# Optimization experiments

Measured on AMD Instinct MI355X. Metric: run time of the kernel, lower is better.

Reference implementation:

```python
import jax, jax.numpy as jnp
import numpy as np

TEMPERATURE = 0.1
EPS = 1e-08
NEG_INF = -9e15


def setup_inputs() -> dict:
    key = jax.random.key(0)
    k1, k2 = jax.random.split(key)
    B, D = 4096, 256
    z_i = jax.random.normal(k1, (B, D), dtype=jnp.float32)
    z_j = jax.random.normal(k2, (B, D), dtype=jnp.float32)
    mask_positive = jnp.ones((B,), dtype=bool)
    return {"z_i": z_i, "z_j": z_j, "mask_positive": mask_positive}


def reference(z_i, z_j, mask_positive):
    B = z_i.shape[0]
    N = 2 * B
    z = jnp.concatenate([z_i, z_j], axis=0)  # [N, D]
    # cosine similarity: normalize (norms clamped to eps) then GEMM
    norms = jnp.maximum(jnp.linalg.norm(z, axis=1, keepdims=True), EPS)
    zn = z / norms
    sim = jnp.matmul(zn, zn.T) / TEMPERATURE  # [N, N]
    # mask self-similarity on diagonal
    rows = jnp.arange(N)
    sim = sim.at[rows, rows].set(NEG_INF)
    logprob = jax.nn.log_softmax(sim, axis=1)
    # positive of row k is row (k+B) mod N
    positives = jnp.concatenate([jnp.arange(B, N), jnp.arange(0, B)])
    loss_vec = -logprob[rows, positives]  # [N]
    mp = jnp.concatenate([mask_positive, mask_positive])  # [N] bool
    cnt = jnp.sum(mp.astype(jnp.float32))
    total = jnp.sum(jnp.where(mp, loss_vec, 0.0))
    loss = jnp.where(cnt > 0, total / jnp.maximum(cnt, 1.0), 0.0)
    return loss
```

## Files before the change

### kernel.cpp

```cpp
#include <hip/hip_runtime.h>
#include <hip/hip_bf16.h>

#define NTOT   8192
#define BHALF  4096
#define DDIM   256
#define TEMP_INV 10.0f
#define SMOD   16
#define NPART  4

typedef __attribute__((ext_vector_type(8))) short bf16x8_t;
typedef __attribute__((ext_vector_type(4))) float f32x4_t;

__device__ inline unsigned short f2bf(float x) {
    __hip_bfloat16 h = __float2bfloat16(x);
    return __builtin_bit_cast(unsigned short, h);
}

__global__ void norm_pair_kernel(const float* __restrict__ zi,
                                 const float* __restrict__ zj,
                                 unsigned short* __restrict__ zn,
                                 float* __restrict__ posdot,
                                 float* __restrict__ s_part) {
    int gtid = blockIdx.x * 256 + threadIdx.x;
    if (gtid < NTOT * NPART) s_part[gtid] = 0.0f;
    int k    = gtid >> 6;
    int lane = gtid & 63;
    float4 vi = reinterpret_cast<const float4*>(zi + (size_t)k * DDIM)[lane];
    float4 vj = reinterpret_cast<const float4*>(zj + (size_t)k * DDIM)[lane];
    float ssi = vi.x*vi.x + vi.y*vi.y + vi.z*vi.z + vi.w*vi.w;
    float ssj = vj.x*vj.x + vj.y*vj.y + vj.z*vj.z + vj.w*vj.w;
    float dot = vi.x*vj.x + vi.y*vj.y + vi.z*vj.z + vi.w*vj.w;
    #pragma unroll
    for (int off = 32; off >= 1; off >>= 1) {
        ssi += __shfl_xor(ssi, off);
        ssj += __shfl_xor(ssj, off);
        dot += __shfl_xor(dot, off);
    }
    float ri = 1.0f / fmaxf(sqrtf(ssi), 1e-8f);
    float rj = 1.0f / fmaxf(sqrtf(ssj), 1e-8f);
    ushort4 oi, oj;
    oi.x = f2bf(vi.x * ri); oi.y = f2bf(vi.y * ri);
    oi.z = f2bf(vi.z * ri); oi.w = f2bf(vi.w * ri);
    oj.x = f2bf(vj.x * rj); oj.y = f2bf(vj.y * rj);
    oj.z = f2bf(vj.z * rj); oj.w = f2bf(vj.w * rj);
    reinterpret_cast<ushort4*>(zn + (size_t)k * DDIM)[lane] = oi;
    reinterpret_cast<ushort4*>(zn + (size_t)(k + BHALF) * DDIM)[lane] = oj;
    if (lane == 0) posdot[k] = dot * ri * rj * TEMP_INV;
}

__global__ void __launch_bounds__(256)
gemm_sym_kernel(const unsigned short* __restrict__ zn,
                float* __restrict__ s_part) {
    __shared__ unsigned short ldsB[64 * 256];
    __shared__ float colred[4][64];

    const int bi = blockIdx.x;
    const int s  = blockIdx.y;
    const int R0 = bi << 7;

    int cs0 = 2 * bi + ((s - 2 * bi) & (SMOD - 1));
    if (cs0 >= 128) return;

    const int tid  = threadIdx.x;
    const int lane = tid & 63;
    const int wv   = tid >> 6;
    const int m    = lane & 15;
    const int quad = lane >> 4;

    float* rowPart = s_part + (size_t)(s  & (NPART - 1)) * NTOT;
    float* colPart = s_part + (size_t)(bi & (NPART - 1)) * NTOT;

    bf16x8_t afrag[2][8];
    #pragma unroll
    for (int rf = 0; rf < 2; ++rf) {
        const unsigned short* arow = zn + (size_t)(R0 + wv*32 + rf*16 + m) * DDIM;
        #pragma unroll
        for (int kk = 0; kk < 8; ++kk)
            afrag[rf][kk] = *reinterpret_cast<const bf16x8_t*>(arow + kk*32 + quad*8);
    }

    float rowacc[2][4] = {{0.f,0.f,0.f,0.f},{0.f,0.f,0.f,0.f}};

    for (int cs = cs0; cs < 128; cs += SMOD) {
        const int C0 = cs << 6;
        const bool isDiag = ((cs >> 1) == bi);

        #pragma unroll
        for (int t = 0; t < 8; ++t) {
            int ci = t * 256 + tid;
            int r = ci >> 5, c = ci & 31;
            bf16x8_t v = *reinterpret_cast<const bf16x8_t*>(
                             zn + (size_t)(C0 + r) * DDIM + c * 8);
            *reinterpret_cast<bf16x8_t*>(&ldsB[r * 256 + ((c ^ (r & 7)) << 3)]) = v;
        }
        __syncthreads();

        #pragma unroll
        for (int cf = 0; cf < 4; ++cf) {
            f32x4_t cacc0 = (f32x4_t){0.f,0.f,0.f,0.f};
            f32x4_t cacc1 = (f32x4_t){0.f,0.f,0.f,0.f};
            #pragma unroll
            for (int kk = 0; kk < 8; ++kk) {
                bf16x8_t b = *reinterpret_cast<const bf16x8_t*>(
                    &ldsB[(cf*16 + m) * 256 + (((kk*4 + quad) ^ (m & 7)) << 3)]);
                cacc0 = __builtin_amdgcn_mfma_f32_16x16x32_bf16(afrag[0][kk], b, cacc0, 0, 0, 0);
                cacc1 = __builtin_amdgcn_mfma_f32_16x16x32_bf16(afrag[1][kk], b, cacc1, 0, 0, 0);
            }
            const int gc = C0 + cf*16 + m;
            float colsum = 0.f;
            #pragma unroll
            for (int r = 0; r < 4; ++r) {
                int gr0 = R0 + wv*32 + quad*4 + r;
                float e0 = __expf(cacc0[r] * TEMP_INV);
                float e1 = __expf(cacc1[r] * TEMP_INV);
                if (isDiag && gr0 == gc)        e0 = 0.f;
                if (isDiag && (gr0 + 16) == gc) e1 = 0.f;
                rowacc[0][r] += e0;
                rowacc[1][r] += e1;
                colsum += e0 + e1;
            }
            if (!isDiag) {
                colsum += __shfl_xor(colsum, 16);
                colsum += __shfl_xor(colsum, 32);
                if (quad == 0) colred[wv][cf*16 + m] = colsum;
            }
        }
        __syncthreads();

        if (!isDiag && tid < 64)
            atomicAdd(&colPart[C0 + tid],
                      colred[0][tid] + colred[1][tid] + colred[2][tid] + colred[3][tid]);
    }

    #pragma unroll
    for (int rf = 0; rf < 2; ++rf)
        #pragma unroll
        for (int r = 0; r < 4; ++r) {
            float v = rowacc[rf][r];
            v += __shfl_xor(v, 1);
            v += __shfl_xor(v, 2);
            v += __shfl_xor(v, 4);
            v += __shfl_xor(v, 8);
            if (m == 0)
                atomicAdd(&rowPart[R0 + wv*32 + rf*16 + quad*4 + r], v);
        }
}

__global__ void finalize_kernel(const float* __restrict__ s_part,
                                const float* __restrict__ posdot,
                                const unsigned char* __restrict__ mask,
                                float* __restrict__ out) {
    int tid = threadIdx.x, lane = tid & 63, wv = tid >> 6;
    float tot = 0.f, cnt = 0.f;
    #pragma unroll
    for (int si = 0; si < NTOT / 1024; ++si) {
        int k = si * 1024 + tid;
        int kb = k & (BHALF - 1);
        if (mask[kb] != 0) {
            float sk = s_part[k] + s_part[NTOT + k]
                     + s_part[2*NTOT + k] + s_part[3*NTOT + k];
            tot += __logf(sk) - posdot[kb];
            cnt += 1.f;
        }
    }
    #pragma unroll
    for (int off = 32; off >= 1; off >>= 1) {
        tot += __shfl_xor(tot, off);
        cnt += __shfl_xor(cnt, off);
    }
    __shared__ float st[16], sc[16];
    if (lane == 0) { st[wv] = tot; sc[wv] = cnt; }
    __syncthreads();
    if (tid == 0) {
        float T = 0.f, C = 0.f;
        #pragma unroll
        for (int i = 0; i < 16; ++i) { T += st[i]; C += sc[i]; }
        out[0] = (C > 0.f) ? (T / fmaxf(C, 1.f)) : 0.f;
    }
}

extern "C" void kernel_launch(void* const* d_in, const int* in_sizes, int n_in,
                              void* d_out, int out_size, void* d_ws, size_t ws_size,
                              hipStream_t stream) {
    const float* zi = (const float*)d_in[0];
    const float* zj = (const float*)d_in[1];
    const unsigned char* mask = (const unsigned char*)d_in[2];
    float* out = (float*)d_out;

    unsigned short* zn = (unsigned short*)d_ws;
    float* s_part = (float*)((char*)d_ws + (size_t)NTOT * DDIM * 2);
    float* posdot = s_part + NPART * NTOT;

    norm_pair_kernel<<<dim3(1024), dim3(256), 0, stream>>>(zi, zj, zn, posdot, s_part);
    gemm_sym_kernel<<<dim3(64, SMOD), dim3(256), 0, stream>>>(zn, s_part);
    finalize_kernel<<<dim3(1), dim3(1024), 0, stream>>>(s_part, posdot, mask, out);
}
```

Before: 111.1 us.

## Pair complementary row blocks per workgroup and read B fragments directly from global

Each workgroup now handles row block bi and its mirror 63-bi, so the triangular work is spread evenly across half as many workgroups. The LDS staging of the B tile and its per-iteration barriers are removed; B fragments are loaded straight from global memory (through cache) into MFMA operands. Column partial sums are buffered in LDS slots and flushed with atomics after a single barrier at the end. Launch bounds request two workgroups per CU. The cost is redundant global/L2 traffic for B, since each wave now fetches the full B tile itself instead of sharing it through LDS.

```diff
diff --git a/kernel.cpp b/kernel.cpp
--- a/kernel.cpp
+++ b/kernel.cpp
@@ -7,6 +7,7 @@
 #define TEMP_INV 10.0f
 #define SMOD   16
 #define NPART  4
+#define MAXSLOT 9
 
 typedef __attribute__((ext_vector_type(8))) short bf16x8_t;
 typedef __attribute__((ext_vector_type(4))) float f32x4_t;
@@ -48,102 +49,112 @@
     if (lane == 0) posdot[k] = dot * ri * rj * TEMP_INV;
 }
 
-__global__ void __launch_bounds__(256)
+__global__ void __launch_bounds__(256, 2)
 gemm_sym_kernel(const unsigned short* __restrict__ zn,
                 float* __restrict__ s_part) {
-    __shared__ unsigned short ldsB[64 * 256];
-    __shared__ float colred[4][64];
-
-    const int bi = blockIdx.x;
-    const int s  = blockIdx.y;
-    const int R0 = bi << 7;
-
-    int cs0 = 2 * bi + ((s - 2 * bi) & (SMOD - 1));
-    if (cs0 >= 128) return;
+    __shared__ float colLDS[MAXSLOT][4][64];
 
     const int tid  = threadIdx.x;
     const int lane = tid & 63;
     const int wv   = tid >> 6;
     const int m    = lane & 15;
     const int quad = lane >> 4;
-
-    float* rowPart = s_part + (size_t)(s  & (NPART - 1)) * NTOT;
-    float* colPart = s_part + (size_t)(bi & (NPART - 1)) * NTOT;
-
-    bf16x8_t afrag[2][8];
-    #pragma unroll
-    for (int rf = 0; rf < 2; ++rf) {
-        const unsigned short* arow = zn + (size_t)(R0 + wv*32 + rf*16 + m) * DDIM;
-        #pragma unroll
-        for (int kk = 0; kk < 8; ++kk)
-            afrag[rf][kk] = *reinterpret_cast<const bf16x8_t*>(arow + kk*32 + quad*8);
-    }
-
-    float rowacc[2][4] = {{0.f,0.f,0.f,0.f},{0.f,0.f,0.f,0.f}};
-
-    for (int cs = cs0; cs < 128; cs += SMOD) {
-        const int C0 = cs << 6;
-        const bool isDiag = ((cs >> 1) == bi);
-
-        #pragma unroll
-        for (int t = 0; t < 8; ++t) {
-            int ci = t * 256 + tid;
-            int r = ci >> 5, c = ci & 31;
-            bf16x8_t v = *reinterpret_cast<const bf16x8_t*>(
-                             zn + (size_t)(C0 + r) * DDIM + c * 8);
-            *reinterpret_cast<bf16x8_t*>(&ldsB[r * 256 + ((c ^ (r & 7)) << 3)]) = v;
-        }
-        __syncthreads();
-
-        #pragma unroll
-        for (int cf = 0; cf < 4; ++cf) {
-            f32x4_t cacc0 = (f32x4_t){0.f,0.f,0.f,0.f};
-            f32x4_t cacc1 = (f32x4_t){0.f,0.f,0.f,0.f};
+    const int biA  = blockIdx.x;
+    const int s    = blockIdx.y;
+
+    float* rowPart = s_part + (size_t)(s   & (NPART - 1)) * NTOT;
+    float* colPart = s_part + (size_t)(biA & (NPART - 1)) * NTOT;
+
+    int slot = 0;
+    #pragma unroll
+    for (int p = 0; p < 2; ++p) {
+        const int bi = p ? (63 - biA) : biA;
+        const int R0 = bi << 7;
+        const int cs0 = 2 * bi + ((s - 2 * bi) & (SMOD - 1));
+        if (cs0 >= 128) continue;
+
+        bf16x8_t afrag[2][8];
+        #pragma unroll
+        for (int rf = 0; rf < 2; ++rf) {
+            const unsigned short* arow = zn + (size_t)(R0 + wv*32 + rf*16 + m) * DDIM;
             #pragma unroll
-            for (int kk = 0; kk < 8; ++kk) {
-                bf16x8_t b = *reinterpret_cast<const bf16x8_t*>(
-                    &ldsB[(cf*16 + m) * 256 + (((kk*4 + quad) ^ (m & 7)) << 3)]);
-                cacc0 = __builtin_amdgcn_mfma_f32_16x16x32_bf16(afrag[0][kk], b, cacc0, 0, 0, 0);
-                cacc1 = __builtin_amdgcn_mfma_f32_16x16x32_bf16(afrag[1][kk], b, cacc1, 0, 0, 0);
+            for (int kk = 0; kk < 8; ++kk)
+                afrag[rf][kk] = *reinterpret_cast<const bf16x8_t*>(arow + kk*32 + quad*8);
+        }
+
+        float rowacc[2][4] = {{0.f,0.f,0.f,0.f},{0.f,0.f,0.f,0.f}};
+
+        for (int cs = cs0; cs < 128; cs += SMOD) {
+            const int C0 = cs << 6;
+            const bool isDiag = ((cs >> 1) == bi);
+
+            #pragma unroll
+            for (int cf = 0; cf < 4; ++cf) {
+                const unsigned short* bbase =
+                    zn + (size_t)(C0 + cf*16 + m) * DDIM + quad*8;
+                f32x4_t c0 = (f32x4_t){0.f,0.f,0.f,0.f};
+                f32x4_t c1 = (f32x4_t){0.f,0.f,0.f,0.f};
+                #pragma unroll
+                for (int kk = 0; kk < 8; ++kk) {
+                    bf16x8_t b = *reinterpret_cast<const bf16x8_t*>(bbase + kk*32);
+                    c0 = __builtin_amdgcn_mfma_f32_16x16x32_bf16(afrag[0][kk], b, c0, 0, 0, 0);
+                    c1 = __builtin_amdgcn_mfma_f32_16x16x32_bf16(afrag[1][kk], b, c1, 0, 0, 0);
+                }
+                const int gc = C0 + cf*16 + m;
+                float colsum = 0.f;
+                #pragma unroll
+                for (int r = 0; r < 4; ++r) {
+                    int gr0 = R0 + wv*32 + quad*4 + r;
+                    float e0 = __expf(c0[r] * TEMP_INV);
+                    float e1 = __expf(c1[r] * TEMP_INV);
+                    if (isDiag && gr0 == gc)        e0 = 0.f;
+                    if (isDiag && (gr0 + 16) == gc) e1 = 0.f;
+                    rowacc[0][r] += e0;
+                    rowacc[1][r] += e1;
+                    colsum += e0 + e1;
+                }
+                if (!isDiag) {
+                    colsum += __shfl_xor(colsum, 16);
+                    colsum += __shfl_xor(colsum, 32);
+                    if (quad == 0) colLDS[slot][wv][cf*16 + m] = colsum;
+                }
             }
-            const int gc = C0 + cf*16 + m;
-            float colsum = 0.f;
+            ++slot;
+        }
+
+        #pragma unroll
+        for (int rf = 0; rf < 2; ++rf)
             #pragma unroll
             for (int r = 0; r < 4; ++r) {
-                int gr0 = R0 + wv*32 + quad*4 + r;
-                float e0 = __expf(cacc0[r] * TEMP_INV);
-                float e1 = __expf(cacc1[r] * TEMP_INV);
-                if (isDiag && gr0 == gc)        e0 = 0.f;
-                if (isDiag && (gr0 + 16) == gc) e1 = 0.f;
-                rowacc[0][r] += e0;
-                rowacc[1][r] += e1;
-                colsum += e0 + e1;
+                float v = rowacc[rf][r];
+                v += __shfl_xor(v, 1);
+                v += __shfl_xor(v, 2);
+                v += __shfl_xor(v, 4);
+                v += __shfl_xor(v, 8);
+                if (m == 0)
+                    atomicAdd(&rowPart[R0 + wv*32 + rf*16 + quad*4 + r], v);
             }
-            if (!isDiag) {
-                colsum += __shfl_xor(colsum, 16);
-                colsum += __shfl_xor(colsum, 32);
-                if (quad == 0) colred[wv][cf*16 + m] = colsum;
+    }
+
+    __syncthreads();
+
+    if (tid < 64) {
+        int slot2 = 0;
+        #pragma unroll
+        for (int p = 0; p < 2; ++p) {
+            const int bi = p ? (63 - biA) : biA;
+            const int cs0 = 2 * bi + ((s - 2 * bi) & (SMOD - 1));
+            if (cs0 >= 128) continue;
+            for (int cs = cs0; cs < 128; cs += SMOD) {
+                if ((cs >> 1) != bi) {
+                    float v = colLDS[slot2][0][tid] + colLDS[slot2][1][tid]
+                            + colLDS[slot2][2][tid] + colLDS[slot2][3][tid];
+                    atomicAdd(&colPart[(cs << 6) + tid], v);
+                }
+                ++slot2;
             }
         }
-        __syncthreads();
-
-        if (!isDiag && tid < 64)
-            atomicAdd(&colPart[C0 + tid],
-                      colred[0][tid] + colred[1][tid] + colred[2][tid] + colred[3][tid]);
-    }
-
-    #pragma unroll
-    for (int rf = 0; rf < 2; ++rf)
-        #pragma unroll
-        for (int r = 0; r < 4; ++r) {
-            float v = rowacc[rf][r];
-            v += __shfl_xor(v, 1);
-            v += __shfl_xor(v, 2);
-            v += __shfl_xor(v, 4);
-            v += __shfl_xor(v, 8);
-            if (m == 0)
-                atomicAdd(&rowPart[R0 + wv*32 + rf*16 + quad*4 + r], v);
-        }
+    }
 }
 
 __global__ void finalize_kernel(const float* __restrict__ s_part,
@@ -192,6 +203,6 @@
     float* posdot = s_part + NPART * NTOT;
 
     norm_pair_kernel<<<dim3(1024), dim3(256), 0, stream>>>(zi, zj, zn, posdot, s_part);
-    gemm_sym_kernel<<<dim3(64, SMOD), dim3(256), 0, stream>>>(zn, s_part);
+    gemm_sym_kernel<<<dim3(32, SMOD), dim3(256), 0, stream>>>(zn, s_part);
     finalize_kernel<<<dim3(1), dim3(1024), 0, stream>>>(s_part, posdot, mask, out);
 }
```

Measured after the change: 144.4 us. 1.3x slower.

## Replace symmetric triangular GEMM with full column-sum GEMM and plain stores

Applied to the files above, without the earlier changes.

Drops the symmetric upper-triangle scheme, which accumulated row and column sums through atomics. Each block now keeps one 64-column slab in LDS and sweeps 2048 rows across four row groups, summing exp only along columns. Results go straight into per-row-group partial buffers, so the atomics and the zero-initialisation in the norm kernel disappear. The exp uses exp2f with a pre-folded scale. The price is roughly double the MFMA and exp work, since symmetry is no longer exploited.

```diff
diff --git a/kernel.cpp b/kernel.cpp
--- a/kernel.cpp
+++ b/kernel.cpp
@@ -4,9 +4,8 @@
 #define NTOT   8192
 #define BHALF  4096
 #define DDIM   256
-#define TEMP_INV 10.0f
-#define SMOD   16
-#define NPART  4
+#define NRG    4
+#define EXPSCALE 14.4269504088896341f
 
 typedef __attribute__((ext_vector_type(8))) short bf16x8_t;
 typedef __attribute__((ext_vector_type(4))) float f32x4_t;
@@ -19,10 +18,8 @@
 __global__ void norm_pair_kernel(const float* __restrict__ zi,
                                  const float* __restrict__ zj,
                                  unsigned short* __restrict__ zn,
-                                 float* __restrict__ posdot,
-                                 float* __restrict__ s_part) {
+                                 float* __restrict__ posdot) {
     int gtid = blockIdx.x * 256 + threadIdx.x;
-    if (gtid < NTOT * NPART) s_part[gtid] = 0.0f;
     int k    = gtid >> 6;
     int lane = gtid & 63;
     float4 vi = reinterpret_cast<const float4*>(zi + (size_t)k * DDIM)[lane];
@@ -45,105 +42,98 @@
     oj.z = f2bf(vj.z * rj); oj.w = f2bf(vj.w * rj);
     reinterpret_cast<ushort4*>(zn + (size_t)k * DDIM)[lane] = oi;
     reinterpret_cast<ushort4*>(zn + (size_t)(k + BHALF) * DDIM)[lane] = oj;
-    if (lane == 0) posdot[k] = dot * ri * rj * TEMP_INV;
+    if (lane == 0) posdot[k] = dot * ri * rj * 10.0f;
 }
 
-__global__ void __launch_bounds__(256)
-gemm_sym_kernel(const unsigned short* __restrict__ zn,
-                float* __restrict__ s_part) {
+__global__ void __launch_bounds__(256, 1)
+gemm_colsum_kernel(const unsigned short* __restrict__ zn,
+                   float* __restrict__ s_part) {
     __shared__ unsigned short ldsB[64 * 256];
-    __shared__ float colred[4][64];
-
-    const int bi = blockIdx.x;
-    const int s  = blockIdx.y;
-    const int R0 = bi << 7;
-
-    int cs0 = 2 * bi + ((s - 2 * bi) & (SMOD - 1));
-    if (cs0 >= 128) return;
+    __shared__ float colLDS[4][64];
 
     const int tid  = threadIdx.x;
     const int lane = tid & 63;
     const int wv   = tid >> 6;
     const int m    = lane & 15;
     const int quad = lane >> 4;
+    const int cs   = blockIdx.x;
+    const int rg   = blockIdx.y;
+    const int C0   = cs << 6;
 
-    float* rowPart = s_part + (size_t)(s  & (NPART - 1)) * NTOT;
-    float* colPart = s_part + (size_t)(bi & (NPART - 1)) * NTOT;
+    #pragma unroll
+    for (int t = 0; t < 8; ++t) {
+        int ci = t * 256 + tid;
+        int r = ci >> 5, c = ci & 31;
+        bf16x8_t v = *reinterpret_cast<const bf16x8_t*>(
+                         zn + (size_t)(C0 + r) * DDIM + c * 8);
+        *reinterpret_cast<bf16x8_t*>(&ldsB[r * 256 + ((c ^ (r & 7)) << 3)]) = v;
+    }
+    __syncthreads();
 
-    bf16x8_t afrag[2][8];
-    #pragma unroll
-    for (int rf = 0; rf < 2; ++rf) {
-        const unsigned short* arow = zn + (size_t)(R0 + wv*32 + rf*16 + m) * DDIM;
+    float expacc[4] = {0.f, 0.f, 0.f, 0.f};
+    const int diagSlab = C0 >> 8;
+
+    for (int rb = 0; rb < 8; ++rb) {
+        const int rowbase = (rg << 11) + (rb << 8);
+        const bool isDiag = ((rowbase >> 8) == diagSlab);
+
+        bf16x8_t afrag[4][8];
         #pragma unroll
-        for (int kk = 0; kk < 8; ++kk)
-            afrag[rf][kk] = *reinterpret_cast<const bf16x8_t*>(arow + kk*32 + quad*8);
-    }
-
-    float rowacc[2][4] = {{0.f,0.f,0.f,0.f},{0.f,0.f,0.f,0.f}};
-
-    for (int cs = cs0; cs < 128; cs += SMOD) {
-        const int C0 = cs << 6;
-        const bool isDiag = ((cs >> 1) == bi);
-
-        #pragma unroll
-        for (int t = 0; t < 8; ++t) {
-            int ci = t * 256 + tid;
-            int r = ci >> 5, c = ci & 31;
-            bf16x8_t v = *reinterpret_cast<const bf16x8_t*>(
-                             zn + (size_t)(C0 + r) * DDIM + c * 8);
-            *reinterpret_cast<bf16x8_t*>(&ldsB[r * 256 + ((c ^ (r & 7)) << 3)]) = v;
+        for (int rf = 0; rf < 4; ++rf) {
+            const unsigned short* arow =
+                zn + (size_t)(rowbase + wv*64 + rf*16 + m) * DDIM;
+            #pragma unroll
+            for (int kk = 0; kk < 8; ++kk)
+                afrag[rf][kk] = *reinterpret_cast<const bf16x8_t*>(arow + kk*32 + quad*8);
         }
-        __syncthreads();
 
         #pragma unroll
         for (int cf = 0; cf < 4; ++cf) {
-            f32x4_t cacc0 = (f32x4_t){0.f,0.f,0.f,0.f};
-            f32x4_t cacc1 = (f32x4_t){0.f,0.f,0.f,0.f};
+            f32x4_t cacc[4];
+            #pragma unroll
+            for (int rf = 0; rf < 4; ++rf) cacc[rf] = (f32x4_t){0.f,0.f,0.f,0.f};
             #pragma unroll
             for (int kk = 0; kk < 8; ++kk) {
                 bf16x8_t b = *reinterpret_cast<const bf16x8_t*>(
                     &ldsB[(cf*16 + m) * 256 + (((kk*4 + quad) ^ (m & 7)) << 3)]);
-                cacc0 = __builtin_amdgcn_mfma_f32_16x16x32_bf16(afrag[0][kk], b, cacc0, 0, 0, 0);
-                cacc1 = __builtin_amdgcn_mfma_f32_16x16x32_bf16(afrag[1][kk], b, cacc1, 0, 0, 0);
+                #pragma unroll
+                for (int rf = 0; rf < 4; ++rf)
+                    cacc[rf] = __builtin_amdgcn_mfma_f32_16x16x32_bf16(
+                        afrag[rf][kk], b, cacc[rf], 0, 0, 0);
             }
             const int gc = C0 + cf*16 + m;
-            float colsum = 0.f;
-            #pragma unroll
-            for (int r = 0; r < 4; ++r) {
-                int gr0 = R0 + wv*32 + quad*4 + r;
-                float e0 = __expf(cacc0[r] * TEMP_INV);
-                float e1 = __expf(cacc1[r] * TEMP_INV);
-                if (isDiag && gr0 == gc)        e0 = 0.f;
-                if (isDiag && (gr0 + 16) == gc) e1 = 0.f;
-                rowacc[0][r] += e0;
-                rowacc[1][r] += e1;
-                colsum += e0 + e1;
+            float acc = expacc[cf];
+            if (isDiag) {
+                #pragma unroll
+                for (int rf = 0; rf < 4; ++rf)
+                    #pragma unroll
+                    for (int r = 0; r < 4; ++r) {
+                        int gr = rowbase + wv*64 + rf*16 + quad*4 + r;
+                        float e = exp2f(cacc[rf][r] * EXPSCALE);
+                        acc += (gr == gc) ? 0.f : e;
+                    }
+            } else {
+                #pragma unroll
+                for (int rf = 0; rf < 4; ++rf)
+                    #pragma unroll
+                    for (int r = 0; r < 4; ++r)
+                        acc += exp2f(cacc[rf][r] * EXPSCALE);
             }
-            if (!isDiag) {
-                colsum += __shfl_xor(colsum, 16);
-                colsum += __shfl_xor(colsum, 32);
-                if (quad == 0) colred[wv][cf*16 + m] = colsum;
-            }
+            expacc[cf] = acc;
         }
-        __syncthreads();
-
-        if (!isDiag && tid < 64)
-            atomicAdd(&colPart[C0 + tid],
-                      colred[0][tid] + colred[1][tid] + colred[2][tid] + colred[3][tid]);
     }
 
     #pragma unroll
-    for (int rf = 0; rf < 2; ++rf)
-        #pragma unroll
-        for (int r = 0; r < 4; ++r) {
-            float v = rowacc[rf][r];
-            v += __shfl_xor(v, 1);
-            v += __shfl_xor(v, 2);
-            v += __shfl_xor(v, 4);
-            v += __shfl_xor(v, 8);
-            if (m == 0)
-                atomicAdd(&rowPart[R0 + wv*32 + rf*16 + quad*4 + r], v);
-        }
+    for (int cf = 0; cf < 4; ++cf) {
+        float v = expacc[cf];
+        v += __shfl_xor(v, 16);
+        v += __shfl_xor(v, 32);
+        if (quad == 0) colLDS[wv][cf*16 + m] = v;
+    }
+    __syncthreads();
+    if (tid < 64)
+        s_part[(size_t)rg * NTOT + C0 + tid] =
+            colLDS[0][tid] + colLDS[1][tid] + colLDS[2][tid] + colLDS[3][tid];
 }
 
 __global__ void finalize_kernel(const float* __restrict__ s_part,
@@ -189,9 +179,9 @@
 
     unsigned short* zn = (unsigned short*)d_ws;
     float* s_part = (float*)((char*)d_ws + (size_t)NTOT * DDIM * 2);
-    float* posdot = s_part + NPART * NTOT;
+    float* posdot = s_part + NRG * NTOT;
 
-    norm_pair_kernel<<<dim3(1024), dim3(256), 0, stream>>>(zi, zj, zn, posdot, s_part);
-    gemm_sym_kernel<<<dim3(64, SMOD), dim3(256), 0, stream>>>(zn, s_part);
+    norm_pair_kernel<<<dim3(1024), dim3(256), 0, stream>>>(zi, zj, zn, posdot);
+    gemm_colsum_kernel<<<dim3(128, NRG), dim3(256), 0, stream>>>(zn, s_part);
     finalize_kernel<<<dim3(1), dim3(1024), 0, stream>>>(s_part, posdot, mask, out);
 }
```

Result: slower. 155.4 us (+39.8%).
